# Kernel tuning notes

Measured on AMD Instinct MI355X. Metric: run time of the kernel, lower is better.

The kernel has to match this reference:

```python
import jax, jax.numpy as jnp
import numpy as np

EPS = 1e-6

def _layernorm(x, gamma, beta):
    mu = jnp.mean(x, axis=-1, keepdims=True)
    var = jnp.mean(jnp.square(x - mu), axis=-1, keepdims=True)
    return (x - mu) * jax.lax.rsqrt(var + EPS) * gamma + beta


def setup_inputs() -> dict:
    key = jax.random.key(0)
    ks = jax.random.split(key, 8)
    B, N, C, F = 2, 2048, 1024, 4096
    s = 0.02
    return {
        "x": jax.random.normal(ks[0], (B, N, C), jnp.float32),
        "Wq": jax.random.normal(ks[1], (C, C), jnp.float32) * s,
        "Wk": jax.random.normal(ks[2], (C, C), jnp.float32) * s,
        "Wv": jax.random.normal(ks[3], (C, C), jnp.float32) * s,
        "Wp": jax.random.normal(ks[4], (C, C), jnp.float32) * s,
        "bp": jnp.zeros((C,), jnp.float32),
        "W1": jax.random.normal(ks[5], (C, F), jnp.float32) * s,
        "b1": jnp.zeros((F,), jnp.float32),
        "W2": jax.random.normal(ks[6], (F, C), jnp.float32) * s,
        "b2": jnp.zeros((C,), jnp.float32),
        "gamma1": jnp.ones((C,), jnp.float32),
        "beta1": jnp.zeros((C,), jnp.float32),
        "gamma2": jnp.ones((C,), jnp.float32),
        "beta2": jnp.zeros((C,), jnp.float32),
    }


def reference(x, Wq, Wk, Wv, Wp, bp, W1, b1, W2, b2, gamma1, beta1, gamma2, beta2):
    B, N, C = x.shape
    H = 16
    D = C // H
    scale = D ** -0.5

    xn = _layernorm(x, gamma1, beta1)
    # QKV projections (no bias); q pre-scaled by head_dim**-0.5 as in source
    q = (xn @ Wq * scale).reshape(B, N, H, D).transpose(0, 2, 1, 3)  # bhnd
    k = (xn @ Wk).reshape(B, N, H, D).transpose(0, 2, 1, 3)
    v = (xn @ Wv).reshape(B, N, H, D).transpose(0, 2, 1, 3)

    attn = jax.nn.softmax(jnp.einsum("bhnd,bhmd->bhnm", q, k), axis=-1)
    y = jnp.einsum("bhnm,bhmd->bhnd", attn, v)
    y = y.transpose(0, 2, 1, 3).reshape(B, N, C)
    x = x + (y @ Wp + bp)

    xn2 = _layernorm(x, gamma2, beta2)
    h = jax.nn.gelu(xn2 @ W1 + b1, approximate=False)  # keras 'gelu' is exact
    x = x + (h @ W2 + b2)
    return x
```

## Files before the change

### kernel.cpp

```cpp
#include <hip/hip_runtime.h>
#include <math.h>

#define BN  4096
#define SEQ 2048
#define CH  1024
#define FF  4096
#define NH  16
#define HD  64

typedef short bf16x8 __attribute__((ext_vector_type(8)));
typedef float f32x4  __attribute__((ext_vector_type(4)));

#define MFMA16(a,b,c) __builtin_amdgcn_mfma_f32_16x16x32_bf16(a,b,c,0,0,0)

__device__ __forceinline__ unsigned short f2b(float f){
  unsigned u = __float_as_uint(f);
  u += 0x7fffu + ((u>>16)&1u);
  return (unsigned short)(u>>16);
}

__device__ __forceinline__ unsigned pk2(float a, float b){
  return __builtin_amdgcn_perm(__float_as_uint(b), __float_as_uint(a), 0x07060302u);
}

#if __has_builtin(__builtin_amdgcn_exp2f)
__device__ __forceinline__ float fexp2(float x){ return __builtin_amdgcn_exp2f(x); }
#else
__device__ __forceinline__ float fexp2(float x){
  float r; asm("v_exp_f32 %0, %1" : "=v"(r) : "v"(x)); return r;
}
#endif

__device__ __forceinline__ void gl2lds16(const void* g, void* l){
  __builtin_amdgcn_global_load_lds(
      (__attribute__((address_space(1))) void*)g,
      (__attribute__((address_space(3))) void*)l, 16, 0, 0);
}

__device__ __forceinline__ unsigned xcd_chunk(unsigned id, unsigned nwg){
  const unsigned cpx = nwg >> 3;
  return (id & 7u)*cpx + (id >> 3);
}

__global__ __launch_bounds__(256) void transpose_all(
    const float* __restrict__ Wq, const float* __restrict__ Wk,
    const float* __restrict__ Wv, const float* __restrict__ Wp,
    const float* __restrict__ W1, const float* __restrict__ W2,
    unsigned short* __restrict__ wq_t, unsigned short* __restrict__ wk_t,
    unsigned short* __restrict__ wv_t, unsigned short* __restrict__ wp_t,
    unsigned short* __restrict__ w1_t, unsigned short* __restrict__ w2_t)
{
  const int id = blockIdx.x;
  const float* in; unsigned short* out; int R, S, bx, by; float scale = 1.f;
  if (id < 1024){
    const int which = id >> 8, t = id & 255;
    bx = t & 15; by = t >> 4; R = 1024; S = 1024;
    if (which == 0){ in = Wq; out = wq_t; scale = 0.18033688011112042f; }
    else if (which == 1){ in = Wk; out = wk_t; }
    else if (which == 2){ in = Wv; out = wv_t; }
    else               { in = Wp; out = wp_t; }
  } else if (id < 2048){
    const int t = id - 1024; bx = t & 63; by = t >> 6;
    R = 1024; S = 4096; in = W1; out = w1_t;
  } else {
    const int t = id - 2048; bx = t & 15; by = t >> 4;
    R = 4096; S = 1024; in = W2; out = w2_t;
  }
  __shared__ float tile[64][65];
  const int tid = threadIdx.x;
  const int tx = tid & 63, ty = tid >> 6;
  const int s0 = bx * 64, r0 = by * 64;
  #pragma unroll
  for (int j = 0; j < 16; j++){
    int r = ty + j*4;
    tile[r][tx] = in[(size_t)(r0 + r)*S + s0 + tx];
  }
  __syncthreads();
  #pragma unroll
  for (int j = 0; j < 16; j++){
    int s = ty + j*4;
    out[(size_t)(s0 + s)*R + r0 + tx] = f2b(tile[tx][s] * scale);
  }
}

__global__ __launch_bounds__(256) void ln_kernel(const float* __restrict__ x,
    const float* __restrict__ gamma, const float* __restrict__ beta,
    unsigned short* __restrict__ out)
{
  const int row = blockIdx.x, tid = threadIdx.x;
  const float4 xv = ((const float4*)(x + (size_t)row*CH))[tid];
  float s  = xv.x + xv.y + xv.z + xv.w;
  float ss = xv.x*xv.x + xv.y*xv.y + xv.z*xv.z + xv.w*xv.w;
  #pragma unroll
  for (int off = 1; off < 64; off <<= 1){
    s  += __shfl_xor(s,  off, 64);
    ss += __shfl_xor(ss, off, 64);
  }
  __shared__ float red[8];
  const int w = tid >> 6;
  if ((tid & 63) == 0){ red[w] = s; red[4+w] = ss; }
  __syncthreads();
  s  = red[0]+red[1]+red[2]+red[3];
  ss = red[4]+red[5]+red[6]+red[7];
  const float mu   = s * (1.f/CH);
  const float rstd = rsqrtf(ss*(1.f/CH) - mu*mu + 1e-6f);
  const float4 g = ((const float4*)gamma)[tid];
  const float4 b = ((const float4*)beta )[tid];
  ushort4 o;
  o.x = f2b((xv.x-mu)*rstd*g.x + b.x);
  o.y = f2b((xv.y-mu)*rstd*g.y + b.y);
  o.z = f2b((xv.z-mu)*rstd*g.z + b.z);
  o.w = f2b((xv.w-mu)*rstd*g.w + b.w);
  ((ushort4*)(out + (size_t)row*CH))[tid] = o;
}

template<int BIAS,int GELU,int RES,int OMODE>
__global__ __launch_bounds__(256,4) void gemm128(const unsigned short* __restrict__ A,
    const unsigned short* __restrict__ Bt, const float* __restrict__ bias,
    const float* __restrict__ resid, float* __restrict__ outF,
    unsigned short* __restrict__ outB, unsigned short* __restrict__ outK,
    unsigned short* __restrict__ outV, int M, int Nn, int K)
{
  __shared__ __align__(16) char lds[32768];
  const int tid = threadIdx.x;
  const int w = tid >> 6, lane = tid & 63;
  const int quad = lane >> 4, l16 = lane & 15;
  const unsigned Wid = xcd_chunk(blockIdx.y*gridDim.x + blockIdx.x,
                                 gridDim.x*gridDim.y);
  const int bx = Wid % gridDim.x, by = Wid / gridDim.x;
  const int m0 = by*128, n0 = bx*128;
  const int wm = (w >> 1)*64, wn = (w & 1)*64;
  f32x4 acc[4][4] = {};
  const int nt = K >> 5;

  const int ci0 = w*2, ci1 = w*2 + 1;
  const int ra0 = ci0*16 + (lane >> 2);
  const int ra1 = ra0 + 16;
  const int ga0 = (lane & 3) ^ ((ra0 >> 1) & 3);
  const int ga1 = (lane & 3) ^ ((ra1 >> 1) & 3);
  const unsigned short* aS0 = A  + (size_t)(m0 + ra0)*K + ga0*8;
  const unsigned short* aS1 = A  + (size_t)(m0 + ra1)*K + ga1*8;
  const unsigned short* bS0 = Bt + (size_t)(n0 + ra0)*K + ga0*8;
  const unsigned short* bS1 = Bt + (size_t)(n0 + ra1)*K + ga1*8;

  auto STAGE = [&](int buf){
    char* Ad = lds + buf*8192;
    char* Bd = lds + 16384 + buf*8192;
    gl2lds16(aS0, Ad + ci0*1024);
    gl2lds16(aS1, Ad + ci1*1024);
    gl2lds16(bS0, Bd + ci0*1024);
    gl2lds16(bS1, Bd + ci1*1024);
    aS0 += 32; aS1 += 32; bS0 += 32; bS1 += 32;
  };

  int aoff[4], boff[4];
  #pragma unroll
  for (int mi = 0; mi < 4; mi++){
    const int r = wm + mi*16 + l16;
    aoff[mi] = r*32 + ((quad ^ ((r >> 1) & 3))*8);
  }
  #pragma unroll
  for (int nj = 0; nj < 4; nj++){
    const int r = wn + nj*16 + l16;
    boff[nj] = r*32 + ((quad ^ ((r >> 1) & 3))*8);
  }

  auto COMPUTE = [&](const unsigned short* Ac, const unsigned short* Bc){
    bf16x8 af[4], bfr[4];
    #pragma unroll
    for (int mi = 0; mi < 4; mi++) af[mi]  = *(const bf16x8*)(Ac + aoff[mi]);
    #pragma unroll
    for (int nj = 0; nj < 4; nj++) bfr[nj] = *(const bf16x8*)(Bc + boff[nj]);
    #pragma unroll
    for (int mi = 0; mi < 4; mi++)
      #pragma unroll
      for (int nj = 0; nj < 4; nj++)
        acc[mi][nj] = MFMA16(af[mi], bfr[nj], acc[mi][nj]);
  };
  const unsigned short* A0 = (const unsigned short*)(lds);
  const unsigned short* A1 = (const unsigned short*)(lds + 8192);
  const unsigned short* B0 = (const unsigned short*)(lds + 16384);
  const unsigned short* B1 = (const unsigned short*)(lds + 24576);

  STAGE(0);
  __syncthreads();
  for (int t2 = 0; t2 < (nt >> 1) - 1; t2++){
    STAGE(1);
    COMPUTE(A0, B0);
    __syncthreads();
    STAGE(0);
    COMPUTE(A1, B1);
    __syncthreads();
  }
  STAGE(1);
  COMPUTE(A0, B0);
  __syncthreads();
  COMPUTE(A1, B1);
  __syncthreads();

  const int colb = n0 + wn;
  const int row0 = m0 + wm;
  if (OMODE == 1 || OMODE == 3){
    unsigned short* scr = (unsigned short*)lds + w*4096;
    const int cg = (OMODE == 3) ? (colb >> 10) : 0;
    #pragma unroll
    for (int nj = 0; nj < 4; nj++){
      const int col = colb + nj*16 + l16;
      const float bv = BIAS ? bias[col] : 0.f;
      #pragma unroll
      for (int mi = 0; mi < 4; mi++){
        #pragma unroll
        for (int r = 0; r < 4; r++){
          const int rl = mi*16 + quad*4 + r;
          float v = acc[mi][nj][r] + bv;
          if (GELU) v = 0.5f*v*(1.f + erff(v*0.70710678118654752f));
          if (RES)  v += resid[(size_t)(row0 + rl)*Nn + col];
          const unsigned short b16 = f2b(v);
          if (OMODE == 3 && cg == 2){
            const int d = nj*16 + l16;
            scr[d*64 + (((rl & 15) << 2) | (rl >> 4))] = b16;
          } else {
            scr[rl*64 + nj*16 + l16] = b16;
          }
        }
      }
    }
    const int sl = (lane & 7)*8;
    #pragma unroll
    for (int j = 0; j < 8; j++){
      const int rr = j*8 + (lane >> 3);
      const bf16x8 vv = *(const bf16x8*)(scr + rr*64 + sl);
      if (OMODE == 1){
        *(bf16x8*)(outB + (size_t)(row0 + rr)*Nn + colb + sl) = vv;
      } else {
        if (cg == 0)
          *(bf16x8*)(outB + (size_t)(row0 + rr)*CH + (colb & (CH-1)) + sl) = vv;
        else if (cg == 1)
          *(bf16x8*)(outK + (size_t)(row0 + rr)*CH + (colb & (CH-1)) + sl) = vv;
        else {
          const int bb = row0 >> 11;
          const int hh = (colb & (CH-1)) >> 6;
          *(bf16x8*)(outV + ((size_t)((bb*NH + hh)*HD) + rr)*SEQ
                          + (row0 & (SEQ-1)) + sl) = vv;
        }
      }
    }
    return;
  }
  #pragma unroll
  for (int nj = 0; nj < 4; nj++){
    const int col = colb + nj*16 + l16;
    const float bv = BIAS ? bias[col] : 0.f;
    #pragma unroll
    for (int mi = 0; mi < 4; mi++){
      #pragma unroll
      for (int r = 0; r < 4; r++){
        const int row = row0 + mi*16 + quad*4 + r;
        float v = acc[mi][nj][r] + bv;
        if (GELU) v = 0.5f*v*(1.f + erff(v*0.70710678118654752f));
        if (RES)  v += resid[(size_t)row*Nn + col];
        outF[(size_t)row*Nn + col] = v;
      }
    }
  }
}

template<int BNT,int BIAS,int GELU,int RES,int OMODE,int SPLITK>
__global__ __launch_bounds__(256,2) void gemm_bt(const unsigned short* __restrict__ A,
    const unsigned short* __restrict__ Bt, const float* __restrict__ bias,
    const float* __restrict__ resid, float* __restrict__ outF,
    unsigned short* __restrict__ outB, unsigned short* __restrict__ outK,
    unsigned short* __restrict__ outV, int M, int Nn, int K)
{
  constexpr int MI  = (BNT==128) ? 4 : 2;
  constexpr int BCH = (BNT==128) ? 4 : 2;
  constexpr int ABYTES = 128*64*2;
  constexpr int BBYTES = BNT*64*2;
  __shared__ __align__(16) char lds[2*ABYTES + 2*BBYTES];
  const int tid = threadIdx.x;
  const int w = tid >> 6, lane = tid & 63;
  const int quad = lane >> 4, l16 = lane & 15;
  const unsigned Wid = xcd_chunk(blockIdx.y*gridDim.x + blockIdx.x,
                                 gridDim.x*gridDim.y);
  const int bx = Wid % gridDim.x, by = Wid / gridDim.x;
  const int m0 = by*128, n0 = bx*BNT;
  const int wm = (BNT==128) ? (w >> 1)*64 : w*32;
  const int wn = (BNT==128) ? (w & 1)*64 : 0;
  const int srow = lane >> 3, sslot = lane & 7;
  f32x4 acc[MI][4] = {};
  const int kseg = SPLITK > 1 ? K / SPLITK : K;
  const int kBeg = SPLITK > 1 ? blockIdx.z * kseg : 0;
  const int nsteps = kseg >> 6;

  auto STAGE = [&](int buf, int k0){
    char* Ad = lds + buf*ABYTES;
    char* Bd = lds + 2*ABYTES + buf*BBYTES;
    #pragma unroll
    for (int i = 0; i < 4; i++){
      const int rb = (w*4 + i)*8;
      const int r = rb + srow;
      const int c = sslot ^ (r & 7);
      gl2lds16(A + (size_t)(m0 + r)*K + k0 + c*8, Ad + rb*128);
    }
    #pragma unroll
    for (int i = 0; i < BCH; i++){
      const int rb = (w*BCH + i)*8;
      const int r = rb + srow;
      const int c = sslot ^ (r & 7);
      gl2lds16(Bt + (size_t)(n0 + r)*K + k0 + c*8, Bd + rb*128);
    }
  };

  STAGE(0, kBeg);
  __syncthreads();
  for (int t = 0; t < nsteps; t++){
    const int cur = t & 1;
    if (t + 1 < nsteps) STAGE(cur ^ 1, kBeg + (t+1)*64);
    const unsigned short* Ac = (const unsigned short*)(lds + cur*ABYTES);
    const unsigned short* Bc = (const unsigned short*)(lds + 2*ABYTES + cur*BBYTES);
    #pragma unroll
    for (int kc = 0; kc < 2; kc++){
      bf16x8 af[MI], bfr[4];
      #pragma unroll
      for (int mi = 0; mi < MI; mi++){
        const int r = wm + mi*16 + l16;
        af[mi] = *(const bf16x8*)(Ac + r*64 + (((kc*4 + quad) ^ (r & 7))*8));
      }
      #pragma unroll
      for (int nj = 0; nj < 4; nj++){
        const int r = wn + nj*16 + l16;
        bfr[nj] = *(const bf16x8*)(Bc + r*64 + (((kc*4 + quad) ^ (r & 7))*8));
      }
      #pragma unroll
      for (int mi = 0; mi < MI; mi++)
        #pragma unroll
        for (int nj = 0; nj < 4; nj++)
          acc[mi][nj] = MFMA16(af[mi], bfr[nj], acc[mi][nj]);
    }
    __syncthreads();
  }

  #pragma unroll
  for (int nj = 0; nj < 4; nj++){
    const int col = n0 + wn + nj*16 + l16;
    const float bv = BIAS ? bias[col] : 0.f;
    #pragma unroll
    for (int mi = 0; mi < MI; mi++){
      #pragma unroll
      for (int r = 0; r < 4; r++){
        const int row = m0 + wm + mi*16 + quad*4 + r;
        float v = acc[mi][nj][r];
        if (SPLITK > 1){
          if (blockIdx.z == 0){
            if (BIAS) v += bias[col];
            if (RES)  v += resid[(size_t)row*Nn + col];
          }
          atomicAdd(&outF[(size_t)row*Nn + col], v);
          continue;
        }
        v += bv;
        if (GELU) v = 0.5f*v*(1.f + erff(v*0.70710678118654752f));
        if (RES)  v += resid[(size_t)row*Nn + col];
        if (OMODE == 0) outF[(size_t)row*Nn + col] = v;
        else outB[(size_t)row*Nn + col] = f2b(v);
      }
    }
  }
}

__global__ __launch_bounds__(256,2) void attn_kernel(const unsigned short* __restrict__ q,
    const unsigned short* __restrict__ k, const unsigned short* __restrict__ vt,
    unsigned short* __restrict__ y)
{
  __shared__ __align__(16) unsigned short Kl[2][64*64];
  __shared__ __align__(16) unsigned short Vl[2][64*64];
  __shared__ __align__(16) unsigned short Pp[4][64*68];
  const int tid = threadIdx.x;
  const int w = tid >> 6, lane = tid & 63;
  const int wq = w & 1, wk = w >> 1;
  const int quad = lane >> 4, l16 = lane & 15;
  const unsigned Wid = xcd_chunk(blockIdx.y*gridDim.x + blockIdx.x,
                                 gridDim.x*gridDim.y);
  const int qt = Wid & 15, bh = Wid >> 4;
  const int b = bh >> 4, h = bh & 15;
  const size_t tb  = ((size_t)b*SEQ)*CH + h*HD;
  const size_t vb_ = (size_t)bh*HD*SEQ;
  const int qr0 = qt*128 + wq*64;

  bf16x8 qf[4][2];
  #pragma unroll
  for (int mi = 0; mi < 4; mi++)
    #pragma unroll
    for (int kc = 0; kc < 2; kc++)
      qf[mi][kc] = *(const bf16x8*)(q + tb + (size_t)(qr0 + mi*16 + l16)*CH + kc*32 + quad*8);

  float sacc[4][4];
  f32x4 o[4][4] = {};
  #pragma unroll
  for (int mi = 0; mi < 4; mi++)
    #pragma unroll
    for (int r = 0; r < 4; r++) sacc[mi][r] = 0.f;

  for (int t = 0; t < 16; t++){
    const int kv0 = wk*1024 + t*64;
    __syncthreads();
    #pragma unroll
    for (int i = 0; i < 8; i++){
      const int r = i*8 + (lane >> 3);
      const int c = (lane & 7) ^ (r & 7);
      if (wq == 0)
        gl2lds16(k  + tb  + (size_t)(kv0 + r)*CH + c*8, (char*)&Kl[wk][0] + i*1024);
      else
        gl2lds16(vt + vb_ + (size_t)r*SEQ + kv0 + c*8, (char*)&Vl[wk][0] + i*1024);
    }
    __syncthreads();

    f32x4 s[4][4] = {};
    __builtin_amdgcn_s_setprio(1);
    #pragma unroll
    for (int kc = 0; kc < 2; kc++){
      #pragma unroll
      for (int nj = 0; nj < 4; nj++){
        bf16x8 kf = *(const bf16x8*)(&Kl[wk][0] + (nj*16 + l16)*64 + (((kc*4 + quad) ^ (l16 & 7))*8));
        #pragma unroll
        for (int mi = 0; mi < 4; mi++)
          s[mi][nj] = MFMA16(qf[mi][kc], kf, s[mi][nj]);
      }
    }
    __builtin_amdgcn_s_setprio(0);
    #pragma unroll
    for (int mi = 0; mi < 4; mi++){
      #pragma unroll
      for (int r = 0; r < 4; r++){
        const float p0 = fexp2(s[mi][0][r]);
        const float p1 = fexp2(s[mi][1][r]);
        const float p2 = fexp2(s[mi][2][r]);
        const float p3 = fexp2(s[mi][3][r]);
        sacc[mi][r] += (p0 + p1) + (p2 + p3);
        uint2 pk;
        pk.x = pk2(p0, p1);
        pk.y = pk2(p2, p3);
        const int prow = mi*16 + quad*4 + r;
        *(uint2*)(&Pp[w][prow*68 + l16*4]) = pk;
      }
    }
    __builtin_amdgcn_s_setprio(1);
    #pragma unroll
    for (int kc = 0; kc < 2; kc++){
      bf16x8 pa[4];
      #pragma unroll
      for (int mi = 0; mi < 4; mi++)
        pa[mi] = *(const bf16x8*)(&Pp[w][(mi*16 + l16)*68 + kc*32 + quad*8]);
      #pragma unroll
      for (int nd = 0; nd < 4; nd++){
        bf16x8 vf = *(const bf16x8*)(&Vl[wk][0] + (nd*16 + l16)*64 + (((kc*4 + quad) ^ (l16 & 7))*8));
        #pragma unroll
        for (int mi = 0; mi < 4; mi++)
          o[mi][nd] = MFMA16(pa[mi], vf, o[mi][nd]);
      }
    }
    __builtin_amdgcn_s_setprio(0);
  }

  __syncthreads();
  float* ob = wq ? (float*)&Vl[0][0] : (float*)&Kl[0][0];
  float* sb = (float*)&Pp[2 + wq][0];
  if (wk == 1){
    #pragma unroll
    for (int mi = 0; mi < 4; mi++)
      #pragma unroll
      for (int nd = 0; nd < 4; nd++)
        #pragma unroll
        for (int r = 0; r < 4; r++){
          const int idx = (mi*4 + nd)*4 + r;
          ob[lane*64 + ((idx + lane) & 63)] = o[mi][nd][r];
        }
    #pragma unroll
    for (int mi = 0; mi < 4; mi++)
      #pragma unroll
      for (int r = 0; r < 4; r++)
        sb[lane*16 + ((mi*4 + r + lane) & 15)] = sacc[mi][r];
  }
  __syncthreads();
  if (wk == 0){
    #pragma unroll
    for (int mi = 0; mi < 4; mi++)
      #pragma unroll
      for (int nd = 0; nd < 4; nd++)
        #pragma unroll
        for (int r = 0; r < 4; r++){
          const int idx = (mi*4 + nd)*4 + r;
          o[mi][nd][r] += ob[lane*64 + ((idx + lane) & 63)];
        }
    #pragma unroll
    for (int mi = 0; mi < 4; mi++){
      #pragma unroll
      for (int r = 0; r < 4; r++){
        float sum = sacc[mi][r] + sb[lane*16 + ((mi*4 + r + lane) & 15)];
        #pragma unroll
        for (int off = 1; off < 16; off <<= 1) sum += __shfl_xor(sum, off, 64);
        const float inv = 1.f / sum;
        const int qr = qr0 + mi*16 + quad*4 + r;
        #pragma unroll
        for (int nd = 0; nd < 4; nd++)
          y[tb + (size_t)qr*CH + nd*16 + l16] = f2b(o[mi][nd][r]*inv);
      }
    }
  }
}

extern "C" void kernel_launch(void* const* d_in, const int* in_sizes, int n_in,
                              void* d_out, int out_size, void* d_ws, size_t ws_size,
                              hipStream_t stream)
{
  (void)in_sizes; (void)n_in; (void)out_size; (void)ws_size;
  const float* x   = (const float*)d_in[0];
  const float* Wq  = (const float*)d_in[1];
  const float* Wk  = (const float*)d_in[2];
  const float* Wv  = (const float*)d_in[3];
  const float* Wp  = (const float*)d_in[4];
  const float* bp  = (const float*)d_in[5];
  const float* W1  = (const float*)d_in[6];
  const float* b1  = (const float*)d_in[7];
  const float* W2  = (const float*)d_in[8];
  const float* b2  = (const float*)d_in[9];
  const float* g1  = (const float*)d_in[10];
  const float* be1 = (const float*)d_in[11];
  const float* g2  = (const float*)d_in[12];
  const float* be2 = (const float*)d_in[13];
  float* out = (float*)d_out;
  char* ws = (char*)d_ws;
  const size_t MB = 1024*1024;
  unsigned short* wq_t = (unsigned short*)(ws +  0*MB);
  unsigned short* wk_t = (unsigned short*)(ws +  2*MB);
  unsigned short* wv_t = (unsigned short*)(ws +  4*MB);
  unsigned short* wp_t = (unsigned short*)(ws +  6*MB);
  unsigned short* w1_t = (unsigned short*)(ws +  8*MB);
  unsigned short* w2_t = (unsigned short*)(ws + 16*MB);
  unsigned short* xn   = (unsigned short*)(ws + 24*MB);
  unsigned short* qb   = (unsigned short*)(ws + 32*MB);
  unsigned short* kb   = (unsigned short*)(ws + 40*MB);
  unsigned short* vtb  = (unsigned short*)(ws + 48*MB);
  unsigned short* yb   = (unsigned short*)(ws + 56*MB);
  float*          x2   = (float*)         (ws + 64*MB);
  unsigned short* xn2  = (unsigned short*)(ws + 80*MB);
  unsigned short* hb   = (unsigned short*)(ws + 88*MB);

  transpose_all<<<dim3(3072),256,0,stream>>>(Wq, Wk, Wv, Wp, W1, W2,
      wq_t, wk_t, wv_t, wp_t, w1_t, w2_t);

  ln_kernel<<<BN,256,0,stream>>>(x, g1, be1, xn);
  gemm128<0,0,0,3><<<dim3(24,32),256,0,stream>>>(xn, wq_t, nullptr, nullptr,
      nullptr, qb, kb, vtb, BN, 3072, CH);
  attn_kernel<<<dim3(16,32),256,0,stream>>>(qb, kb, vtb, yb);
  gemm_bt<64,1,0,1,0,0><<<dim3(16,32),256,0,stream>>>(yb, wp_t, bp, x, x2,
      nullptr, nullptr, nullptr, BN, CH, CH);
  ln_kernel<<<BN,256,0,stream>>>(x2, g2, be2, xn2);
  gemm128<1,1,0,1><<<dim3(32,32),256,0,stream>>>(xn2, w1_t, b1, nullptr, nullptr,
      hb, nullptr, nullptr, BN, FF, CH);
  gemm_bt<64,1,0,1,0,0><<<dim3(16,32),256,0,stream>>>(hb, w2_t, b2, x2, out,
      nullptr, nullptr, nullptr, BN, CH, FF);
}
```

Measured before the change: 325.3 us.

## Add 256x128 FFN1 GEMM tile, 2D XCD-aware block remap, hoisted staging pointers

```diff
diff --git a/kernel.cpp b/kernel.cpp
--- a/kernel.cpp
+++ b/kernel.cpp
@@ -40,6 +40,18 @@
 __device__ __forceinline__ unsigned xcd_chunk(unsigned id, unsigned nwg){
   const unsigned cpx = nwg >> 3;
   return (id & 7u)*cpx + (id >> 3);
+}
+
+__device__ __forceinline__ void xcd2d(int gx, int rx, int ry, int xin,
+                                      int& bx, int& by){
+  const unsigned d = blockIdx.y*gx + blockIdx.x;
+  const unsigned k = d & 7u, j = d >> 3;
+  const unsigned nrx = (unsigned)gx / (unsigned)rx;
+  const unsigned kx = k % nrx, ky = k / nrx;
+  unsigned lx, ly;
+  if (xin){ lx = j % (unsigned)rx; ly = j / (unsigned)rx; }
+  else    { ly = j % (unsigned)ry; lx = j / (unsigned)ry; }
+  bx = kx*rx + lx; by = ky*ry + ly;
 }
 
 __global__ __launch_bounds__(256) void transpose_all(
@@ -119,15 +131,14 @@
     const unsigned short* __restrict__ Bt, const float* __restrict__ bias,
     const float* __restrict__ resid, float* __restrict__ outF,
     unsigned short* __restrict__ outB, unsigned short* __restrict__ outK,
-    unsigned short* __restrict__ outV, int M, int Nn, int K)
+    unsigned short* __restrict__ outV, int M, int Nn, int K,
+    int rx, int ry, int xin)
 {
   __shared__ __align__(16) char lds[32768];
   const int tid = threadIdx.x;
   const int w = tid >> 6, lane = tid & 63;
   const int quad = lane >> 4, l16 = lane & 15;
-  const unsigned Wid = xcd_chunk(blockIdx.y*gridDim.x + blockIdx.x,
-                                 gridDim.x*gridDim.y);
-  const int bx = Wid % gridDim.x, by = Wid / gridDim.x;
+  int bx, by; xcd2d(gridDim.x, rx, ry, xin, bx, by);
   const int m0 = by*128, n0 = bx*128;
   const int wm = (w >> 1)*64, wn = (w & 1)*64;
   f32x4 acc[4][4] = {};
@@ -265,12 +276,155 @@
   }
 }
 
+template<int BIAS,int GELU,int RES,int OMODE>
+__global__ __launch_bounds__(256,2) void gemm256x128(const unsigned short* __restrict__ A,
+    const unsigned short* __restrict__ Bt, const float* __restrict__ bias,
+    const float* __restrict__ resid, float* __restrict__ outF,
+    unsigned short* __restrict__ outB, int M, int Nn, int K,
+    int rx, int ry, int xin)
+{
+  __shared__ __align__(16) char lds[49152];
+  const int tid = threadIdx.x;
+  const int w = tid >> 6, lane = tid & 63;
+  const int quad = lane >> 4, l16 = lane & 15;
+  int bx, by; xcd2d(gridDim.x, rx, ry, xin, bx, by);
+  const int m0 = by*256, n0 = bx*128;
+  const int wm = (w >> 1)*128, wn = (w & 1)*64;
+  f32x4 acc[8][4] = {};
+  const int nt = K >> 5;
+
+  const int sr = lane >> 2, ss = lane & 3;
+  const unsigned short* aP[4];
+  const unsigned short* bP[2];
+  int aD[4], bD[2];
+  #pragma unroll
+  for (int i = 0; i < 4; i++){
+    const int ci = w*4 + i;
+    const int r = ci*16 + sr;
+    const int g = ss ^ ((r >> 1) & 3);
+    aP[i] = A + (size_t)(m0 + r)*K + g*8;
+    aD[i] = ci*1024;
+  }
+  #pragma unroll
+  for (int i = 0; i < 2; i++){
+    const int ci = w*2 + i;
+    const int r = ci*16 + sr;
+    const int g = ss ^ ((r >> 1) & 3);
+    bP[i] = Bt + (size_t)(n0 + r)*K + g*8;
+    bD[i] = ci*1024;
+  }
+
+  auto STAGE = [&](int buf){
+    char* Ad = lds + buf*24576;
+    char* Bd = Ad + 16384;
+    #pragma unroll
+    for (int i = 0; i < 4; i++){ gl2lds16(aP[i], Ad + aD[i]); aP[i] += 32; }
+    #pragma unroll
+    for (int i = 0; i < 2; i++){ gl2lds16(bP[i], Bd + bD[i]); bP[i] += 32; }
+  };
+
+  int aoff[8], boff[4];
+  #pragma unroll
+  for (int mf = 0; mf < 8; mf++){
+    const int r = wm + mf*16 + l16;
+    aoff[mf] = r*32 + ((quad ^ ((r >> 1) & 3))*8);
+  }
+  #pragma unroll
+  for (int nj = 0; nj < 4; nj++){
+    const int r = wn + nj*16 + l16;
+    boff[nj] = r*32 + ((quad ^ ((r >> 1) & 3))*8);
+  }
+
+  auto COMPUTE = [&](const unsigned short* Ac, const unsigned short* Bc){
+    bf16x8 af[8], bfr[4];
+    #pragma unroll
+    for (int mf = 0; mf < 8; mf++) af[mf]  = *(const bf16x8*)(Ac + aoff[mf]);
+    #pragma unroll
+    for (int nj = 0; nj < 4; nj++) bfr[nj] = *(const bf16x8*)(Bc + boff[nj]);
+    #pragma unroll
+    for (int mf = 0; mf < 8; mf++)
+      #pragma unroll
+      for (int nj = 0; nj < 4; nj++)
+        acc[mf][nj] = MFMA16(af[mf], bfr[nj], acc[mf][nj]);
+  };
+  const unsigned short* A0 = (const unsigned short*)(lds);
+  const unsigned short* A1 = (const unsigned short*)(lds + 24576);
+  const unsigned short* B0 = (const unsigned short*)(lds + 16384);
+  const unsigned short* B1 = (const unsigned short*)(lds + 40960);
+
+  STAGE(0);
+  __syncthreads();
+  for (int t2 = 0; t2 < (nt >> 1) - 1; t2++){
+    STAGE(1);
+    COMPUTE(A0, B0);
+    __syncthreads();
+    STAGE(0);
+    COMPUTE(A1, B1);
+    __syncthreads();
+  }
+  STAGE(1);
+  COMPUTE(A0, B0);
+  __syncthreads();
+  COMPUTE(A1, B1);
+  __syncthreads();
+
+  const int colb = n0 + wn;
+  const int row0 = m0 + wm;
+  if (OMODE == 1){
+    unsigned short* scr = (unsigned short*)lds + w*4096;
+    #pragma unroll
+    for (int h = 0; h < 2; h++){
+      #pragma unroll
+      for (int nj = 0; nj < 4; nj++){
+        const int col = colb + nj*16 + l16;
+        const float bv = BIAS ? bias[col] : 0.f;
+        #pragma unroll
+        for (int mi = 0; mi < 4; mi++){
+          #pragma unroll
+          for (int r = 0; r < 4; r++){
+            const int rl = mi*16 + quad*4 + r;
+            float v = acc[h*4 + mi][nj][r] + bv;
+            if (GELU) v = 0.5f*v*(1.f + erff(v*0.70710678118654752f));
+            if (RES)  v += resid[(size_t)(row0 + h*64 + rl)*Nn + col];
+            scr[rl*64 + nj*16 + l16] = f2b(v);
+          }
+        }
+      }
+      const int sl = (lane & 7)*8;
+      #pragma unroll
+      for (int j = 0; j < 8; j++){
+        const int rr = j*8 + (lane >> 3);
+        *(bf16x8*)(outB + (size_t)(row0 + h*64 + rr)*Nn + colb + sl) =
+            *(const bf16x8*)(scr + rr*64 + sl);
+      }
+    }
+    return;
+  }
+  #pragma unroll
+  for (int nj = 0; nj < 4; nj++){
+    const int col = colb + nj*16 + l16;
+    const float bv = BIAS ? bias[col] : 0.f;
+    #pragma unroll
+    for (int mf = 0; mf < 8; mf++){
+      #pragma unroll
+      for (int r = 0; r < 4; r++){
+        const int row = row0 + mf*16 + quad*4 + r;
+        float v = acc[mf][nj][r] + bv;
+        if (GELU) v = 0.5f*v*(1.f + erff(v*0.70710678118654752f));
+        if (RES)  v += resid[(size_t)row*Nn + col];
+        outF[(size_t)row*Nn + col] = v;
+      }
+    }
+  }
+}
+
 template<int BNT,int BIAS,int GELU,int RES,int OMODE,int SPLITK>
 __global__ __launch_bounds__(256,2) void gemm_bt(const unsigned short* __restrict__ A,
     const unsigned short* __restrict__ Bt, const float* __restrict__ bias,
     const float* __restrict__ resid, float* __restrict__ outF,
     unsigned short* __restrict__ outB, unsigned short* __restrict__ outK,
-    unsigned short* __restrict__ outV, int M, int Nn, int K)
+    unsigned short* __restrict__ outV, int M, int Nn, int K,
+    int rx, int ry, int xin)
 {
   constexpr int MI  = (BNT==128) ? 4 : 2;
   constexpr int BCH = (BNT==128) ? 4 : 2;
@@ -280,9 +434,7 @@
   const int tid = threadIdx.x;
   const int w = tid >> 6, lane = tid & 63;
   const int quad = lane >> 4, l16 = lane & 15;
-  const unsigned Wid = xcd_chunk(blockIdx.y*gridDim.x + blockIdx.x,
-                                 gridDim.x*gridDim.y);
-  const int bx = Wid % gridDim.x, by = Wid / gridDim.x;
+  int bx, by; xcd2d(gridDim.x, rx, ry, xin, bx, by);
   const int m0 = by*128, n0 = bx*BNT;
   const int wm = (BNT==128) ? (w >> 1)*64 : w*32;
   const int wn = (BNT==128) ? (w & 1)*64 : 0;
@@ -292,53 +444,78 @@
   const int kBeg = SPLITK > 1 ? blockIdx.z * kseg : 0;
   const int nsteps = kseg >> 6;
 
-  auto STAGE = [&](int buf, int k0){
+  const unsigned short* aP[4];
+  const unsigned short* bP[BCH];
+  int aD[4], bD[BCH];
+  #pragma unroll
+  for (int i = 0; i < 4; i++){
+    const int rb = (w*4 + i)*8;
+    aP[i] = A + (size_t)(m0 + rb + srow)*K + kBeg + (sslot ^ srow)*8;
+    aD[i] = rb*128;
+  }
+  #pragma unroll
+  for (int i = 0; i < BCH; i++){
+    const int rb = (w*BCH + i)*8;
+    bP[i] = Bt + (size_t)(n0 + rb + srow)*K + kBeg + (sslot ^ srow)*8;
+    bD[i] = rb*128;
+  }
+  auto STAGE = [&](int buf){
     char* Ad = lds + buf*ABYTES;
     char* Bd = lds + 2*ABYTES + buf*BBYTES;
     #pragma unroll
-    for (int i = 0; i < 4; i++){
-      const int rb = (w*4 + i)*8;
-      const int r = rb + srow;
-      const int c = sslot ^ (r & 7);
-      gl2lds16(A + (size_t)(m0 + r)*K + k0 + c*8, Ad + rb*128);
-    }
-    #pragma unroll
-    for (int i = 0; i < BCH; i++){
-      const int rb = (w*BCH + i)*8;
-      const int r = rb + srow;
-      const int c = sslot ^ (r & 7);
-      gl2lds16(Bt + (size_t)(n0 + r)*K + k0 + c*8, Bd + rb*128);
-    }
+    for (int i = 0; i < 4; i++){ gl2lds16(aP[i], Ad + aD[i]); aP[i] += 64; }
+    #pragma unroll
+    for (int i = 0; i < BCH; i++){ gl2lds16(bP[i], Bd + bD[i]); bP[i] += 64; }
   };
 
-  STAGE(0, kBeg);
-  __syncthreads();
-  for (int t = 0; t < nsteps; t++){
-    const int cur = t & 1;
-    if (t + 1 < nsteps) STAGE(cur ^ 1, kBeg + (t+1)*64);
-    const unsigned short* Ac = (const unsigned short*)(lds + cur*ABYTES);
-    const unsigned short* Bc = (const unsigned short*)(lds + 2*ABYTES + cur*BBYTES);
+  int aoff[2][MI], boff[2][4];
+  #pragma unroll
+  for (int kc = 0; kc < 2; kc++){
+    #pragma unroll
+    for (int mi = 0; mi < MI; mi++){
+      const int r = wm + mi*16 + l16;
+      aoff[kc][mi] = r*64 + (((kc*4 + quad) ^ (r & 7))*8);
+    }
+    #pragma unroll
+    for (int nj = 0; nj < 4; nj++){
+      const int r = wn + nj*16 + l16;
+      boff[kc][nj] = r*64 + (((kc*4 + quad) ^ (r & 7))*8);
+    }
+  }
+  auto COMPUTE = [&](const unsigned short* Ac, const unsigned short* Bc){
     #pragma unroll
     for (int kc = 0; kc < 2; kc++){
       bf16x8 af[MI], bfr[4];
       #pragma unroll
-      for (int mi = 0; mi < MI; mi++){
-        const int r = wm + mi*16 + l16;
-        af[mi] = *(const bf16x8*)(Ac + r*64 + (((kc*4 + quad) ^ (r & 7))*8));
-      }
-      #pragma unroll
-      for (int nj = 0; nj < 4; nj++){
-        const int r = wn + nj*16 + l16;
-        bfr[nj] = *(const bf16x8*)(Bc + r*64 + (((kc*4 + quad) ^ (r & 7))*8));
-      }
+      for (int mi = 0; mi < MI; mi++) af[mi]  = *(const bf16x8*)(Ac + aoff[kc][mi]);
+      #pragma unroll
+      for (int nj = 0; nj < 4; nj++) bfr[nj] = *(const bf16x8*)(Bc + boff[kc][nj]);
       #pragma unroll
       for (int mi = 0; mi < MI; mi++)
         #pragma unroll
         for (int nj = 0; nj < 4; nj++)
           acc[mi][nj] = MFMA16(af[mi], bfr[nj], acc[mi][nj]);
     }
+  };
+  const unsigned short* A0 = (const unsigned short*)(lds);
+  const unsigned short* A1 = (const unsigned short*)(lds + ABYTES);
+  const unsigned short* B0 = (const unsigned short*)(lds + 2*ABYTES);
+  const unsigned short* B1 = (const unsigned short*)(lds + 2*ABYTES + BBYTES);
+
+  STAGE(0);
+  __syncthreads();
+  for (int t2 = 0; t2 < (nsteps >> 1) - 1; t2++){
+    STAGE(1);
+    COMPUTE(A0, B0);
     __syncthreads();
-  }
+    STAGE(0);
+    COMPUTE(A1, B1);
+    __syncthreads();
+  }
+  STAGE(1);
+  COMPUTE(A0, B0);
+  __syncthreads();
+  COMPUTE(A1, B1);
 
   #pragma unroll
   for (int nj = 0; nj < 4; nj++){
@@ -551,13 +728,13 @@
 
   ln_kernel<<<BN,256,0,stream>>>(x, g1, be1, xn);
   gemm128<0,0,0,3><<<dim3(24,32),256,0,stream>>>(xn, wq_t, nullptr, nullptr,
-      nullptr, qb, kb, vtb, BN, 3072, CH);
+      nullptr, qb, kb, vtb, BN, 3072, CH, 12, 8, 0);
   attn_kernel<<<dim3(16,32),256,0,stream>>>(qb, kb, vtb, yb);
   gemm_bt<64,1,0,1,0,0><<<dim3(16,32),256,0,stream>>>(yb, wp_t, bp, x, x2,
-      nullptr, nullptr, nullptr, BN, CH, CH);
+      nullptr, nullptr, nullptr, BN, CH, CH, 8, 8, 0);
   ln_kernel<<<BN,256,0,stream>>>(x2, g2, be2, xn2);
-  gemm128<1,1,0,1><<<dim3(32,32),256,0,stream>>>(xn2, w1_t, b1, nullptr, nullptr,
-      hb, nullptr, nullptr, BN, FF, CH);
+  gemm256x128<1,1,0,1><<<dim3(32,16),256,0,stream>>>(xn2, w1_t, b1, nullptr,
+      nullptr, hb, BN, FF, CH, 16, 4, 0);
   gemm_bt<64,1,0,1,0,0><<<dim3(16,32),256,0,stream>>>(hb, w2_t, b2, x2, out,
-      nullptr, nullptr, nullptr, BN, CH, FF);
-}
+      nullptr, nullptr, nullptr, BN, CH, FF, 8, 8, 1);
+}
```

New measurement: 331.1 us. No clear change (+1.8%).

## Add 256x256 eight-wave pipelined GEMM for FFN up-projection with GELU

Applied to the files above, without the earlier changes.

```diff
diff --git a/kernel.cpp b/kernel.cpp
--- a/kernel.cpp
+++ b/kernel.cpp
@@ -112,6 +112,167 @@
   o.z = f2b((xv.z-mu)*rstd*g.z + b.z);
   o.w = f2b((xv.w-mu)*rstd*g.w + b.w);
   ((ushort4*)(out + (size_t)row*CH))[tid] = o;
+}
+
+__global__ __launch_bounds__(512,2) void gemm8p(const unsigned short* __restrict__ A,
+    const unsigned short* __restrict__ Bt, const float* __restrict__ bias,
+    unsigned short* __restrict__ outB, int M, int Nn, int K)
+{
+  __shared__ __align__(16) char lds[131072];
+  const int tid = threadIdx.x;
+  const int w = tid >> 6, lane = tid & 63;
+  const int quad = lane >> 4, l16 = lane & 15;
+  const unsigned Wid = xcd_chunk(blockIdx.y*gridDim.x + blockIdx.x,
+                                 gridDim.x*gridDim.y);
+  const int bx = Wid % gridDim.x, by = Wid / gridDim.x;
+  const int m0 = by*256, n0 = bx*256;
+  const int wm = (w >> 2)*128, wn = (w & 3)*64;
+  f32x4 acc[8][4] = {};
+  const int nt = K >> 6;
+
+  const int srow = w*8 + (lane >> 3);
+  const int schunk = (lane & 7) ^ ((lane >> 3) & 7);
+  const int dwv = (w*8)*128;
+  const unsigned short* pA0a = A  + (size_t)(m0 +   0 + srow)*K + schunk*8;
+  const unsigned short* pA0b = A  + (size_t)(m0 + 128 + srow)*K + schunk*8;
+  const unsigned short* pA1a = A  + (size_t)(m0 +  64 + srow)*K + schunk*8;
+  const unsigned short* pA1b = A  + (size_t)(m0 + 192 + srow)*K + schunk*8;
+  const unsigned short* pB1a = Bt + (size_t)(n0 +   0 + srow)*K + schunk*8;
+  const unsigned short* pB1b = Bt + (size_t)(n0 +  64 + srow)*K + schunk*8;
+  const unsigned short* pB2a = Bt + (size_t)(n0 + 128 + srow)*K + schunk*8;
+  const unsigned short* pB2b = Bt + (size_t)(n0 + 192 + srow)*K + schunk*8;
+  char* const ldsA = lds;
+  char* const ldsB = lds + 65536;
+
+  auto stB1 = [&](int buf){ char* d = ldsB + buf*32768 + dwv;
+    gl2lds16(pB1a, d);            gl2lds16(pB1b, d + 64*128);
+    pB1a += 64; pB1b += 64; };
+  auto stB2 = [&](int buf){ char* d = ldsB + buf*32768 + dwv;
+    gl2lds16(pB2a, d + 128*128);  gl2lds16(pB2b, d + 192*128);
+    pB2a += 64; pB2b += 64; };
+  auto stA0 = [&](int buf){ char* d = ldsA + buf*32768 + dwv;
+    gl2lds16(pA0a, d);            gl2lds16(pA0b, d + 128*128);
+    pA0a += 64; pA0b += 64; };
+  auto stA1 = [&](int buf){ char* d = ldsA + buf*32768 + dwv;
+    gl2lds16(pA1a, d + 64*128);   gl2lds16(pA1b, d + 192*128);
+    pA1a += 64; pA1b += 64; };
+
+  const int ch0 = ((quad)     ^ (l16 & 7))*8;
+  const int ch1 = ((4 + quad) ^ (l16 & 7))*8;
+
+  stB1(0); stB2(0); stA0(0); stA1(0); stB1(1);
+  asm volatile("s_waitcnt vmcnt(4)" ::: "memory");
+  asm volatile("s_barrier" ::: "memory");
+
+  bf16x8 af[4][2], bfA[2][2], bfB[2][2];
+  for (int kt = 0; kt < nt; kt++){
+    const unsigned short* Ac = (const unsigned short*)(ldsA + (kt & 1)*32768);
+    const unsigned short* Bc = (const unsigned short*)(ldsB + (kt & 1)*32768);
+    const int nb = (kt + 1) & 1;
+    #pragma unroll
+    for (int mi = 0; mi < 4; mi++){
+      const int r = (wm + mi*16 + l16)*64;
+      af[mi][0] = *(const bf16x8*)(Ac + r + ch0);
+      af[mi][1] = *(const bf16x8*)(Ac + r + ch1);
+    }
+    #pragma unroll
+    for (int nj = 0; nj < 2; nj++){
+      const int r = (wn + nj*16 + l16)*64;
+      bfA[nj][0] = *(const bf16x8*)(Bc + r + ch0);
+      bfA[nj][1] = *(const bf16x8*)(Bc + r + ch1);
+    }
+    if (kt + 1 < nt) stB2(nb);
+    asm volatile("s_barrier" ::: "memory");
+    asm volatile("s_waitcnt lgkmcnt(0)" ::: "memory");
+    __builtin_amdgcn_s_setprio(1);
+    #pragma unroll
+    for (int mi = 0; mi < 4; mi++)
+      #pragma unroll
+      for (int nj = 0; nj < 2; nj++){
+        acc[mi][nj] = MFMA16(af[mi][0], bfA[nj][0], acc[mi][nj]);
+        acc[mi][nj] = MFMA16(af[mi][1], bfA[nj][1], acc[mi][nj]);
+      }
+    __builtin_amdgcn_s_setprio(0);
+    asm volatile("s_barrier" ::: "memory");
+    #pragma unroll
+    for (int nj = 0; nj < 2; nj++){
+      const int r = (wn + 32 + nj*16 + l16)*64;
+      bfB[nj][0] = *(const bf16x8*)(Bc + r + ch0);
+      bfB[nj][1] = *(const bf16x8*)(Bc + r + ch1);
+    }
+    if (kt + 1 < nt) stA0(nb);
+    if (kt < nt - 1) asm volatile("s_waitcnt vmcnt(6)" ::: "memory");
+    else             asm volatile("s_waitcnt vmcnt(0)" ::: "memory");
+    asm volatile("s_barrier" ::: "memory");
+    asm volatile("s_waitcnt lgkmcnt(0)" ::: "memory");
+    __builtin_amdgcn_s_setprio(1);
+    #pragma unroll
+    for (int mi = 0; mi < 4; mi++)
+      #pragma unroll
+      for (int nj = 0; nj < 2; nj++){
+        acc[mi][2+nj] = MFMA16(af[mi][0], bfB[nj][0], acc[mi][2+nj]);
+        acc[mi][2+nj] = MFMA16(af[mi][1], bfB[nj][1], acc[mi][2+nj]);
+      }
+    __builtin_amdgcn_s_setprio(0);
+    asm volatile("s_barrier" ::: "memory");
+    #pragma unroll
+    for (int mi = 0; mi < 4; mi++){
+      const int r = (wm + 64 + mi*16 + l16)*64;
+      af[mi][0] = *(const bf16x8*)(Ac + r + ch0);
+      af[mi][1] = *(const bf16x8*)(Ac + r + ch1);
+    }
+    if (kt + 1 < nt) stA1(nb);
+    asm volatile("s_barrier" ::: "memory");
+    asm volatile("s_waitcnt lgkmcnt(0)" ::: "memory");
+    __builtin_amdgcn_s_setprio(1);
+    #pragma unroll
+    for (int mi = 0; mi < 4; mi++)
+      #pragma unroll
+      for (int nj = 0; nj < 2; nj++){
+        acc[4+mi][2+nj] = MFMA16(af[mi][0], bfB[nj][0], acc[4+mi][2+nj]);
+        acc[4+mi][2+nj] = MFMA16(af[mi][1], bfB[nj][1], acc[4+mi][2+nj]);
+      }
+    __builtin_amdgcn_s_setprio(0);
+    asm volatile("s_barrier" ::: "memory");
+    if (kt + 2 < nt) stB1(kt & 1);
+    if (kt < nt - 2)       asm volatile("s_waitcnt vmcnt(4)" ::: "memory");
+    else if (kt == nt - 2) asm volatile("s_waitcnt vmcnt(2)" ::: "memory");
+    asm volatile("s_barrier" ::: "memory");
+    __builtin_amdgcn_s_setprio(1);
+    #pragma unroll
+    for (int mi = 0; mi < 4; mi++)
+      #pragma unroll
+      for (int nj = 0; nj < 2; nj++){
+        acc[4+mi][nj] = MFMA16(af[mi][0], bfA[nj][0], acc[4+mi][nj]);
+        acc[4+mi][nj] = MFMA16(af[mi][1], bfA[nj][1], acc[4+mi][nj]);
+      }
+    __builtin_amdgcn_s_setprio(0);
+    asm volatile("s_barrier" ::: "memory");
+  }
+
+  const int colb = n0 + wn, row0 = m0 + wm;
+  unsigned short* scr = (unsigned short*)lds + w*8192;
+  #pragma unroll
+  for (int nj = 0; nj < 4; nj++){
+    const float bv = bias[colb + nj*16 + l16];
+    #pragma unroll
+    for (int mf = 0; mf < 8; mf++){
+      #pragma unroll
+      for (int r = 0; r < 4; r++){
+        const int rl = mf*16 + quad*4 + r;
+        float v = acc[mf][nj][r] + bv;
+        v = 0.5f*v*(1.f + erff(v*0.70710678118654752f));
+        scr[rl*64 + nj*16 + l16] = f2b(v);
+      }
+    }
+  }
+  const int sl = (lane & 7)*8;
+  #pragma unroll
+  for (int j = 0; j < 16; j++){
+    const int rr = j*8 + (lane >> 3);
+    *(bf16x8*)(outB + (size_t)(row0 + rr)*Nn + colb + sl) =
+        *(const bf16x8*)(scr + rr*64 + sl);
+  }
 }
 
 template<int BIAS,int GELU,int RES,int OMODE>
@@ -556,8 +717,7 @@
   gemm_bt<64,1,0,1,0,0><<<dim3(16,32),256,0,stream>>>(yb, wp_t, bp, x, x2,
       nullptr, nullptr, nullptr, BN, CH, CH);
   ln_kernel<<<BN,256,0,stream>>>(x2, g2, be2, xn2);
-  gemm128<1,1,0,1><<<dim3(32,32),256,0,stream>>>(xn2, w1_t, b1, nullptr, nullptr,
-      hb, nullptr, nullptr, BN, FF, CH);
+  gemm8p<<<dim3(16,16),512,0,stream>>>(xn2, w1_t, b1, hb, BN, FF, CH);
   gemm_bt<64,1,0,1,0,0><<<dim3(16,32),256,0,stream>>>(hb, w2_t, b2, x2, out,
       nullptr, nullptr, nullptr, BN, CH, FF);
 }
```

Result: no change. 326.2 us (+0.3%).
